# Kernel tuning notes

Measured on AMD Instinct MI355X. Metric: run time of the kernel, lower is better.

The kernel has to match this reference:

```python
import jax, jax.numpy as jnp
import numpy as np

N = 50000
E = 800000
IN_DIM = 512
HID = 512
MLP_HID = 200
N_CLASSES = 2
BN_EPS = 1e-5


def setup_inputs() -> dict:
    key = jax.random.key(0)
    ks = jax.random.split(key, 12)
    def glorot(k, shape):
        fan_in, fan_out = shape[0], shape[1]
        lim = (6.0 / (fan_in + fan_out)) ** 0.5
        return jax.random.uniform(k, shape, jnp.float32, -lim, lim)
    return {
        "features": jax.random.normal(ks[0], (N, IN_DIM), jnp.float32),
        "src": jax.random.randint(ks[1], (E,), 0, N),
        "dst": jax.random.randint(ks[2], (E,), 0, N),
        # SAGEConv layer 1 & 2 (gcn aggregator -> only fc_neigh)
        "W1": glorot(ks[3], (IN_DIM, HID)),
        "b1": jnp.zeros((HID,), jnp.float32),
        "W2": glorot(ks[4], (HID, HID)),
        "b2": jnp.zeros((HID,), jnp.float32),
        # MLP predictor: Linear -> ReLU -> BatchNorm1d -> Linear
        "Wh": glorot(ks[5], (HID, MLP_HID)),
        "bh": jnp.zeros((MLP_HID,), jnp.float32),
        "gamma": jnp.ones((MLP_HID,), jnp.float32),
        "beta": jnp.zeros((MLP_HID,), jnp.float32),
        "Wo": glorot(ks[6], (MLP_HID, N_CLASSES)),
        "bo": jnp.zeros((N_CLASSES,), jnp.float32),
    }


def _sage_gcn_layer(h, src, dst, deg, W, b):
    # dgl.add_self_loop(g) + SAGEConv(aggregator_type='gcn'):
    # neigh_sum over (edges + self-loop) = segment_sum + h;
    # gcn aggregator then adds h_self once more and divides by (in_deg_with_selfloop + 1):
    #   h_neigh = (segment_sum(h[src]) + 2*h) / (deg_orig + 2)
    agg = jax.ops.segment_sum(h[src], dst, num_segments=h.shape[0])
    h_neigh = (agg + 2.0 * h) / (deg + 2.0)[:, None]
    # fc_neigh then activation=relu (fc commutes with the convex aggregation,
    # applied post-aggregation for clarity)
    return jax.nn.relu(h_neigh @ W + b)


def reference(features, src, dst, W1, b1, W2, b2, Wh, bh, gamma, beta, Wo, bo):
    n = features.shape[0]
    deg = jax.ops.segment_sum(jnp.ones_like(src, dtype=features.dtype), dst, num_segments=n)
    h = _sage_gcn_layer(features, src, dst, deg, W1, b1)  # dropout = identity (eval)
    h = _sage_gcn_layer(h, src, dst, deg, W2, b2)
    # MLP predictor (dropout identity): Linear -> ReLU -> BatchNorm1d -> Linear
    h = jax.nn.relu(h @ Wh + bh)
    mean = jnp.mean(h, axis=0)
    var = jnp.var(h, axis=0)  # biased var, matching torch BatchNorm training fwd
    h = (h - mean) * jax.lax.rsqrt(var + BN_EPS) * gamma + beta
    return h @ Wo + bo
```

## Files before the change

### kernel.cpp

```cpp
#include <hip/hip_runtime.h>

#define NN 50000
#define NE 800000
#define DIM 512
#define MLPH 200

typedef __attribute__((ext_vector_type(8))) short short8;
typedef __attribute__((ext_vector_type(4))) float f32x4;
typedef __attribute__((ext_vector_type(4))) unsigned int u32x4;

#define GL2LDS(g, l)                                                     \
    __builtin_amdgcn_global_load_lds(                                    \
        (const __attribute__((address_space(1))) unsigned int*)(g),      \
        (__attribute__((address_space(3))) unsigned int*)(l), 16, 0, 0)

__device__ inline unsigned short f2bf(float f) {
    unsigned int u = __float_as_uint(f);
    unsigned int r = (u + 0x7fffu + ((u >> 16) & 1u)) >> 16;
    return (unsigned short)r;
}
__device__ inline float bflo(unsigned u) { return __uint_as_float(u << 16); }
__device__ inline float bfhi(unsigned u) { return __uint_as_float(u & 0xffff0000u); }
__device__ inline float bf1(unsigned short u) { return __uint_as_float((unsigned)u << 16); }
__device__ inline unsigned pack2(float a, float b) {
    return (unsigned)f2bf(a) | ((unsigned)f2bf(b) << 16);
}

__global__ void k_hist(const int* __restrict__ dst, int* __restrict__ counts) {
    int e = blockIdx.x * blockDim.x + threadIdx.x;
    if (e < NE) atomicAdd(&counts[dst[e]], 1);
}

__global__ void k_part(const int* __restrict__ counts, int* __restrict__ partial) {
    int t = threadIdx.x;
    int i = blockIdx.x * 256 + t;
    int x = (i < NN) ? counts[i] : 0;
#pragma unroll
    for (int off = 32; off; off >>= 1) x += __shfl_down(x, off);
    __shared__ int ws[4];
    if ((t & 63) == 0) ws[t >> 6] = x;
    __syncthreads();
    if (t == 0) partial[blockIdx.x] = ws[0] + ws[1] + ws[2] + ws[3];
}

__global__ void k_scanp(int* __restrict__ partial, int* __restrict__ rowstart, int nb) {
    __shared__ int ws[4];
    int t = threadIdx.x;
    int x = (t < nb) ? partial[t] : 0;
    int v = x;
#pragma unroll
    for (int off = 1; off < 64; off <<= 1) {
        int u = __shfl_up(v, off);
        if ((t & 63) >= off) v += u;
    }
    if ((t & 63) == 63) ws[t >> 6] = v;
    __syncthreads();
    int add = 0;
#pragma unroll
    for (int w = 0; w < 4; w++)
        if (w < (t >> 6)) add += ws[w];
    if (t < nb) partial[t] = v - x + add;
    if (t == 255) rowstart[NN] = v + add;
}

__global__ void k_scan2(const int* __restrict__ counts, const int* __restrict__ pexcl,
                        int* __restrict__ rowstart, int* __restrict__ cursor) {
    __shared__ int ws[4];
    int t = threadIdx.x;
    int i = blockIdx.x * 256 + t;
    int x = (i < NN) ? counts[i] : 0;
    int v = x;
#pragma unroll
    for (int off = 1; off < 64; off <<= 1) {
        int u = __shfl_up(v, off);
        if ((t & 63) >= off) v += u;
    }
    if ((t & 63) == 63) ws[t >> 6] = v;
    __syncthreads();
    int add = 0;
#pragma unroll
    for (int w = 0; w < 4; w++)
        if (w < (t >> 6)) add += ws[w];
    if (i < NN) {
        int r = pexcl[blockIdx.x] + v - x + add;
        rowstart[i] = r;
        cursor[i] = r;
    }
}

__global__ void k_fill(const int* __restrict__ src, const int* __restrict__ dst,
                       int* __restrict__ cursor, int* __restrict__ adj) {
    int e = blockIdx.x * blockDim.x + threadIdx.x;
    if (e < NE) {
        int p = atomicAdd(&cursor[dst[e]], 1);
        adj[p] = src[e];
    }
}

__global__ void k_cvt(const float* __restrict__ in, ushort* __restrict__ out, int n4) {
    int i = blockIdx.x * blockDim.x + threadIdx.x;
    if (i >= n4) return;
    float4 v = *(const float4*)(in + (size_t)i * 4);
    ushort2 a{f2bf(v.x), f2bf(v.y)}, b{f2bf(v.z), f2bf(v.w)};
    *(ushort2*)(out + (size_t)i * 4) = a;
    *(ushort2*)(out + (size_t)i * 4 + 2) = b;
}

__global__ void k_wt3(const float* __restrict__ W1, const float* __restrict__ W2,
                      const float* __restrict__ Wh, ushort* __restrict__ W1t,
                      ushort* __restrict__ W2t, ushort* __restrict__ Wht) {
    int i = blockIdx.x * 256 + threadIdx.x;
    const int S1 = 512 * 512, S2 = 2 * 512 * 512, S3 = 2 * 512 * 512 + MLPH * 512;
    if (i < S1) {
        int n = i >> 9, k = i & 511;
        W1t[i] = f2bf(W1[(size_t)k * 512 + n]);
    } else if (i < S2) {
        int j = i - S1, n = j >> 9, k = j & 511;
        W2t[j] = f2bf(W2[(size_t)k * 512 + n]);
    } else if (i < S3) {
        int j = i - S2, n = j >> 9, k = j & 511;
        Wht[j] = f2bf(Wh[(size_t)k * MLPH + n]);
    }
}

__device__ inline void addrow(float* acc, uint4 v) {
    acc[0] += bflo(v.x); acc[1] += bfhi(v.x);
    acc[2] += bflo(v.y); acc[3] += bfhi(v.y);
    acc[4] += bflo(v.z); acc[5] += bfhi(v.z);
    acc[6] += bflo(v.w); acc[7] += bfhi(v.w);
}

__global__ __launch_bounds__(256) void k_agg_bf(const ushort* __restrict__ h,
                                                const int* __restrict__ rowstart,
                                                const int* __restrict__ adj,
                                                ushort* __restrict__ out) {
    int node = blockIdx.x * 4 + (threadIdx.x >> 6);
    int lane = threadIdx.x & 63;
    if (node >= NN) return;
    int s = rowstart[node], e = rowstart[node + 1];
    const size_t coff = (size_t)lane * 8;
    float acc[8];
    {
        uint4 v = *(const uint4*)(h + (size_t)node * DIM + coff);
        acc[0] = 2.f * bflo(v.x); acc[1] = 2.f * bfhi(v.x);
        acc[2] = 2.f * bflo(v.y); acc[3] = 2.f * bfhi(v.y);
        acc[4] = 2.f * bflo(v.z); acc[5] = 2.f * bfhi(v.z);
        acc[6] = 2.f * bflo(v.w); acc[7] = 2.f * bfhi(v.w);
    }
    int i = s;
    int e4 = s + ((e - s) & ~3);
    for (; i < e4; i += 4) {
        int n0 = adj[i], n1 = adj[i + 1], n2 = adj[i + 2], n3 = adj[i + 3];
        uint4 v0 = *(const uint4*)(h + (size_t)n0 * DIM + coff);
        uint4 v1 = *(const uint4*)(h + (size_t)n1 * DIM + coff);
        uint4 v2 = *(const uint4*)(h + (size_t)n2 * DIM + coff);
        uint4 v3 = *(const uint4*)(h + (size_t)n3 * DIM + coff);
        addrow(acc, v0);
        addrow(acc, v1);
        addrow(acc, v2);
        addrow(acc, v3);
    }
    for (; i < e; i++) {
        int nbr = adj[i];
        uint4 v = *(const uint4*)(h + (size_t)nbr * DIM + coff);
        addrow(acc, v);
    }
    float inv = 1.0f / (float)(e - s + 2);
    u32x4 o;
    o.x = pack2(acc[0] * inv, acc[1] * inv);
    o.y = pack2(acc[2] * inv, acc[3] * inv);
    o.z = pack2(acc[4] * inv, acc[5] * inv);
    o.w = pack2(acc[6] * inv, acc[7] * inv);
    __builtin_nontemporal_store(o, (u32x4*)(out + (size_t)node * DIM + coff));
}

template <int NCOLS, int OMODE>
__global__ __launch_bounds__(512) void k_ggemm(const ushort* __restrict__ A,
                                               const ushort* __restrict__ Bt,
                                               const float* __restrict__ bias,
                                               float* __restrict__ Cf,
                                               ushort* __restrict__ Cb, int M) {
    constexpr int K = 512;
    constexpr int NT = K / 32;
    constexpr int NC = (NCOLS + 127) / 128;
    __shared__ ushort As[3][256 * 32];
    __shared__ ushort Bs[3][128 * 32];
    const int tid = threadIdx.x;
    const int wid = tid >> 6, lane = tid & 63;
    const int wm = wid >> 1, wn = wid & 1;

    const int cpx = gridDim.x >> 3;
    const int wg = (blockIdx.x & 7) * cpx + (blockIdx.x >> 3);
    const int col0 = (wg % NC) * 128;
    const int row0 = (wg / NC) * 256;

    const int l15 = lane & 15, lk = (lane >> 4) * 8;
    const int lrow = lane >> 2;
    const int lseg = (lane & 3) * 8;

    auto stage = [&](int buf, int k0) {
#pragma unroll
        for (int j = 0; j < 2; j++) {
            const int r = wid * 16 + j * 128;
            int gr = row0 + r + lrow;
            if (gr > M - 1) gr = M - 1;
            GL2LDS(A + (size_t)gr * K + k0 + lseg, &As[buf][r * 32]);
        }
        const int rb = wid * 16;
        int gc = col0 + rb + lrow;
        if (NCOLS % 128 != 0) {
            if (gc > NCOLS - 1) gc = NCOLS - 1;
        }
        GL2LDS(Bt + (size_t)gc * K + k0 + lseg, &Bs[buf][rb * 32]);
    };

    f32x4 acc[4][4] = {};
    stage(0, 0);
    stage(1, 32);
    asm volatile("s_waitcnt vmcnt(3)" ::: "memory");
    __builtin_amdgcn_s_barrier();

    for (int t = 0; t < NT; ++t) {
        const int cur = t % 3;
        if (t + 2 < NT) stage((t + 2) % 3, (t + 2) * 32);
        short8 a[4], b[4];
#pragma unroll
        for (int m = 0; m < 4; m++)
            a[m] = *(const short8*)(&As[cur][(wm * 64 + m * 16 + l15) * 32 + lk]);
#pragma unroll
        for (int n = 0; n < 4; n++)
            b[n] = *(const short8*)(&Bs[cur][(wn * 64 + n * 16 + l15) * 32 + lk]);
#pragma unroll
        for (int m = 0; m < 4; m++)
#pragma unroll
            for (int n = 0; n < 4; n++)
                acc[m][n] = __builtin_amdgcn_mfma_f32_16x16x32_bf16(a[m], b[n], acc[m][n], 0, 0, 0);
        if (t + 2 < NT) {
            asm volatile("s_waitcnt vmcnt(3)" ::: "memory");
            __builtin_amdgcn_s_barrier();
        } else if (t + 1 < NT) {
            asm volatile("s_waitcnt vmcnt(0)" ::: "memory");
            __builtin_amdgcn_s_barrier();
        }
    }

    const int crow = row0 + wm * 64;
    const int ccol = col0 + wn * 64;
#pragma unroll
    for (int n = 0; n < 4; n++) {
        int c = ccol + n * 16 + l15;
        if (NCOLS % 128 != 0 && c >= NCOLS) continue;
        float bv = bias[c];
#pragma unroll
        for (int m = 0; m < 4; m++) {
#pragma unroll
            for (int i = 0; i < 4; i++) {
                int r = crow + m * 16 + (lane >> 4) * 4 + i;
                if (r >= M) continue;
                float v = fmaxf(acc[m][n][i] + bv, 0.0f);
                if (OMODE == 0) Cf[(size_t)r * NCOLS + c] = v;
                else Cb[(size_t)r * NCOLS + c] = f2bf(v);
            }
        }
    }
}

__global__ void k_bnstat(const ushort* __restrict__ hm, float* __restrict__ gsum,
                         float* __restrict__ gsq) {
    int j = threadIdx.x;
    if (j >= MLPH) return;
    float s = 0.f, q = 0.f;
    for (int r = blockIdx.x; r < NN; r += gridDim.x) {
        float v = bf1(hm[(size_t)r * MLPH + j]);
        s += v;
        q += v * v;
    }
    atomicAdd(&gsum[j], s);
    atomicAdd(&gsq[j], q);
}

__global__ void k_bnfin(const float* __restrict__ gsum, const float* __restrict__ gsq,
                        const float* __restrict__ gamma, const float* __restrict__ beta,
                        const float* __restrict__ Wo, const float* __restrict__ bo,
                        float* __restrict__ Wo2, float* __restrict__ bo2) {
    __shared__ float sh[MLPH];
    int j = threadIdx.x;
    if (j < MLPH) {
        float mean = gsum[j] / (float)NN;
        float var = gsq[j] / (float)NN - mean * mean;
        float scale = gamma[j] * rsqrtf(var + 1e-5f);
        float shift = beta[j] - mean * scale;
        sh[j] = shift;
        Wo2[j * 2 + 0] = scale * Wo[j * 2 + 0];
        Wo2[j * 2 + 1] = scale * Wo[j * 2 + 1];
    }
    __syncthreads();
    if (j < 2) {
        float acc = bo[j];
        for (int t = 0; t < MLPH; t++) acc += sh[t] * Wo[t * 2 + j];
        bo2[j] = acc;
    }
}

__global__ void k_out(const ushort* __restrict__ hm, const float* __restrict__ Wo2,
                      const float* __restrict__ bo2, float* __restrict__ out) {
    __shared__ float w[MLPH * 2];
    if (threadIdx.x < MLPH * 2) w[threadIdx.x] = Wo2[threadIdx.x];
    __syncthreads();
    int wid = (blockIdx.x * blockDim.x + threadIdx.x) >> 6;
    int lane = threadIdx.x & 63;
    if (wid >= NN) return;
    const ushort* row = hm + (size_t)wid * MLPH;
    float p0 = 0.f, p1 = 0.f;
    for (int j = lane; j < MLPH; j += 64) {
        float v = bf1(row[j]);
        p0 += v * w[j * 2 + 0];
        p1 += v * w[j * 2 + 1];
    }
    for (int off = 32; off; off >>= 1) {
        p0 += __shfl_down(p0, off);
        p1 += __shfl_down(p1, off);
    }
    if (lane == 0) {
        out[wid * 2 + 0] = p0 + bo2[0];
        out[wid * 2 + 1] = p1 + bo2[1];
    }
}

extern "C" void kernel_launch(void* const* d_in, const int* in_sizes, int n_in,
                              void* d_out, int out_size, void* d_ws, size_t ws_size,
                              hipStream_t stream) {
    const float* features = (const float*)d_in[0];
    const int* src = (const int*)d_in[1];
    const int* dst = (const int*)d_in[2];
    const float* W1 = (const float*)d_in[3];
    const float* b1 = (const float*)d_in[4];
    const float* W2 = (const float*)d_in[5];
    const float* b2 = (const float*)d_in[6];
    const float* Wh = (const float*)d_in[7];
    const float* bh = (const float*)d_in[8];
    const float* gamma = (const float*)d_in[9];
    const float* beta = (const float*)d_in[10];
    const float* Wo = (const float*)d_in[11];
    const float* bo = (const float*)d_in[12];
    float* out = (float*)d_out;

    char* w = (char*)d_ws;
    auto alloc = [&](size_t bytes) -> void* {
        void* p = (void*)w;
        w += (bytes + 255) & ~(size_t)255;
        return p;
    };
    ushort* fb = (ushort*)alloc((size_t)NN * DIM * 2);
    ushort* ab = (ushort*)alloc((size_t)NN * DIM * 2);
    ushort* hb = (ushort*)alloc((size_t)NN * DIM * 2);
    ushort* W1t = (ushort*)alloc((size_t)DIM * DIM * 2);
    ushort* W2t = (ushort*)alloc((size_t)DIM * DIM * 2);
    ushort* Wht = (ushort*)alloc((size_t)MLPH * DIM * 2);
    int* adj = (int*)alloc((size_t)NE * 4);
    int* counts = (int*)alloc((size_t)NN * 4);
    int* rowstart = (int*)alloc((size_t)(NN + 1) * 4);
    int* cursor = (int*)alloc((size_t)NN * 4);
    int* partial = (int*)alloc(256 * 4);
    float* gsum = (float*)alloc(MLPH * 4);
    float* gsq = (float*)alloc(MLPH * 4);
    float* Wo2 = (float*)alloc(MLPH * 2 * 4);
    float* bo2 = (float*)alloc(2 * 4);

    hipMemsetAsync(counts, 0, (size_t)NN * 4, stream);
    hipMemsetAsync(gsum, 0, MLPH * 4, stream);
    hipMemsetAsync(gsq, 0, MLPH * 4, stream);

    const int NB = (NN + 255) / 256;

    k_hist<<<(NE + 255) / 256, 256, 0, stream>>>(dst, counts);
    k_part<<<NB, 256, 0, stream>>>(counts, partial);
    k_scanp<<<1, 256, 0, stream>>>(partial, rowstart, NB);
    k_scan2<<<NB, 256, 0, stream>>>(counts, partial, rowstart, cursor);
    k_fill<<<(NE + 255) / 256, 256, 0, stream>>>(src, dst, cursor, adj);

    const int n4 = NN * DIM / 4;
    k_cvt<<<(n4 + 255) / 256, 256, 0, stream>>>(features, fb, n4);
    const int WT = 2 * 512 * 512 + MLPH * 512;
    k_wt3<<<(WT + 255) / 256, 256, 0, stream>>>(W1, W2, Wh, W1t, W2t, Wht);

    const int MBr = (NN + 255) / 256;
    const int G512 = 4 * MBr;
    const int G200 = 2 * MBr;

    k_agg_bf<<<(NN + 3) / 4, 256, 0, stream>>>(fb, rowstart, adj, ab);
    k_ggemm<DIM, 1><<<G512, 512, 0, stream>>>(ab, W1t, b1, nullptr, hb, NN);
    k_agg_bf<<<(NN + 3) / 4, 256, 0, stream>>>(hb, rowstart, adj, ab);
    k_ggemm<DIM, 1><<<G512, 512, 0, stream>>>(ab, W2t, b2, nullptr, fb, NN);
    k_ggemm<MLPH, 1><<<G200, 512, 0, stream>>>(fb, Wht, bh, nullptr, ab, NN);
    k_bnstat<<<512, 256, 0, stream>>>(ab, gsum, gsq);
    k_bnfin<<<1, 256, 0, stream>>>(gsum, gsq, gamma, beta, Wo, bo, Wo2, bo2);
    k_out<<<(NN * 64 + 511) / 512, 512, 0, stream>>>(ab, Wo2, bo2, out);
}
```

Measured before the change: 591.4 us.

## Fuse neighbor aggregation with layer GEMM via shared-memory tile

Replaces the separate aggregation kernel and tiled GEMM with one kernel per SAGE layer. Each block aggregates 64 node rows into an LDS tile, then multiplies that tile by the transposed weights with MFMA, reading B directly from global memory. This removes the round-trip of the aggregated matrix through HBM and one launch per layer. In exchange it gives up the LDS-staged, pipelined B loads of the original GEMM, and the aggregation phase runs serially before the compute phase. The output is written as scalar bf16 stores. The aggregation gather loop is also unrolled by 8 instead of 4.

```diff
diff --git a/kernel.cpp b/kernel.cpp
--- a/kernel.cpp
+++ b/kernel.cpp
@@ -130,48 +130,101 @@
     acc[6] += bflo(v.w); acc[7] += bfhi(v.w);
 }
 
-__global__ __launch_bounds__(256) void k_agg_bf(const ushort* __restrict__ h,
-                                                const int* __restrict__ rowstart,
-                                                const int* __restrict__ adj,
-                                                ushort* __restrict__ out) {
-    int node = blockIdx.x * 4 + (threadIdx.x >> 6);
-    int lane = threadIdx.x & 63;
-    if (node >= NN) return;
-    int s = rowstart[node], e = rowstart[node + 1];
-    const size_t coff = (size_t)lane * 8;
-    float acc[8];
+__global__ __launch_bounds__(512) void k_fused(const ushort* __restrict__ h,
+                                               const int* __restrict__ rowstart,
+                                               const int* __restrict__ adj,
+                                               const ushort* __restrict__ Bt,
+                                               const float* __restrict__ bias,
+                                               ushort* __restrict__ C, int M) {
+    constexpr int K = 512;
+    constexpr int LDP = 520;
+    __shared__ ushort P[64 * LDP];
+    const int tid = threadIdx.x;
+    const int wid = tid >> 6, lane = tid & 63;
+    const int row0 = blockIdx.x * 64;
+
     {
-        uint4 v = *(const uint4*)(h + (size_t)node * DIM + coff);
-        acc[0] = 2.f * bflo(v.x); acc[1] = 2.f * bfhi(v.x);
-        acc[2] = 2.f * bflo(v.y); acc[3] = 2.f * bfhi(v.y);
-        acc[4] = 2.f * bflo(v.z); acc[5] = 2.f * bfhi(v.z);
-        acc[6] = 2.f * bflo(v.w); acc[7] = 2.f * bfhi(v.w);
-    }
-    int i = s;
-    int e4 = s + ((e - s) & ~3);
-    for (; i < e4; i += 4) {
-        int n0 = adj[i], n1 = adj[i + 1], n2 = adj[i + 2], n3 = adj[i + 3];
-        uint4 v0 = *(const uint4*)(h + (size_t)n0 * DIM + coff);
-        uint4 v1 = *(const uint4*)(h + (size_t)n1 * DIM + coff);
-        uint4 v2 = *(const uint4*)(h + (size_t)n2 * DIM + coff);
-        uint4 v3 = *(const uint4*)(h + (size_t)n3 * DIM + coff);
-        addrow(acc, v0);
-        addrow(acc, v1);
-        addrow(acc, v2);
-        addrow(acc, v3);
-    }
-    for (; i < e; i++) {
-        int nbr = adj[i];
-        uint4 v = *(const uint4*)(h + (size_t)nbr * DIM + coff);
-        addrow(acc, v);
-    }
-    float inv = 1.0f / (float)(e - s + 2);
-    u32x4 o;
-    o.x = pack2(acc[0] * inv, acc[1] * inv);
-    o.y = pack2(acc[2] * inv, acc[3] * inv);
-    o.z = pack2(acc[4] * inv, acc[5] * inv);
-    o.w = pack2(acc[6] * inv, acc[7] * inv);
-    __builtin_nontemporal_store(o, (u32x4*)(out + (size_t)node * DIM + coff));
+        const size_t coff = (size_t)lane * 8;
+        for (int i = 0; i < 8; i++) {
+            const int prow = wid * 8 + i;
+            int node = row0 + prow;
+            const int nd = (node < M) ? node : (M - 1);
+            const int s = rowstart[nd], e = rowstart[nd + 1];
+            float acc[8];
+            {
+                uint4 v = *(const uint4*)(h + (size_t)nd * DIM + coff);
+                acc[0] = 2.f * bflo(v.x); acc[1] = 2.f * bfhi(v.x);
+                acc[2] = 2.f * bflo(v.y); acc[3] = 2.f * bfhi(v.y);
+                acc[4] = 2.f * bflo(v.z); acc[5] = 2.f * bfhi(v.z);
+                acc[6] = 2.f * bflo(v.w); acc[7] = 2.f * bfhi(v.w);
+            }
+            int j = s;
+            int e8 = s + ((e - s) & ~7);
+            for (; j < e8; j += 8) {
+                uint4 v0 = *(const uint4*)(h + (size_t)adj[j + 0] * DIM + coff);
+                uint4 v1 = *(const uint4*)(h + (size_t)adj[j + 1] * DIM + coff);
+                uint4 v2 = *(const uint4*)(h + (size_t)adj[j + 2] * DIM + coff);
+                uint4 v3 = *(const uint4*)(h + (size_t)adj[j + 3] * DIM + coff);
+                uint4 v4 = *(const uint4*)(h + (size_t)adj[j + 4] * DIM + coff);
+                uint4 v5 = *(const uint4*)(h + (size_t)adj[j + 5] * DIM + coff);
+                uint4 v6 = *(const uint4*)(h + (size_t)adj[j + 6] * DIM + coff);
+                uint4 v7 = *(const uint4*)(h + (size_t)adj[j + 7] * DIM + coff);
+                addrow(acc, v0); addrow(acc, v1); addrow(acc, v2); addrow(acc, v3);
+                addrow(acc, v4); addrow(acc, v5); addrow(acc, v6); addrow(acc, v7);
+            }
+            for (; j < e; j++) {
+                uint4 v = *(const uint4*)(h + (size_t)adj[j] * DIM + coff);
+                addrow(acc, v);
+            }
+            float inv = 1.0f / (float)(e - s + 2);
+            u32x4 o;
+            o.x = pack2(acc[0] * inv, acc[1] * inv);
+            o.y = pack2(acc[2] * inv, acc[3] * inv);
+            o.z = pack2(acc[4] * inv, acc[5] * inv);
+            o.w = pack2(acc[6] * inv, acc[7] * inv);
+            *(u32x4*)(&P[prow * LDP + lane * 8]) = o;
+        }
+    }
+    __syncthreads();
+
+    const int wm = wid >> 2;
+    const int wn = wid & 3;
+    const int l15 = lane & 15, lk = (lane >> 4) * 8;
+    const ushort* bbase = Bt + (size_t)(wn * 128) * K;
+
+    f32x4 acc[2][8] = {};
+    for (int k0 = 0; k0 < K; k0 += 32) {
+        short8 b[8];
+#pragma unroll
+        for (int n = 0; n < 8; n++)
+            b[n] = *(const short8*)(bbase + (size_t)(n * 16 + l15) * K + k0 + lk);
+        short8 a[2];
+#pragma unroll
+        for (int m = 0; m < 2; m++)
+            a[m] = *(const short8*)(&P[(wm * 32 + m * 16 + l15) * LDP + k0 + lk]);
+#pragma unroll
+        for (int m = 0; m < 2; m++)
+#pragma unroll
+            for (int n = 0; n < 8; n++)
+                acc[m][n] = __builtin_amdgcn_mfma_f32_16x16x32_bf16(a[m], b[n], acc[m][n], 0, 0, 0);
+    }
+
+    const int crow = row0 + wm * 32;
+    const int ccol = wn * 128;
+#pragma unroll
+    for (int n = 0; n < 8; n++) {
+        int c = ccol + n * 16 + l15;
+        float bv = bias[c];
+#pragma unroll
+        for (int m = 0; m < 2; m++) {
+#pragma unroll
+            for (int i = 0; i < 4; i++) {
+                int r = crow + m * 16 + (lane >> 4) * 4 + i;
+                if (r >= M) continue;
+                C[(size_t)r * 512 + c] = f2bf(fmaxf(acc[m][n][i] + bv, 0.0f));
+            }
+        }
+    }
 }
 
 template <int NCOLS, int OMODE>
@@ -352,8 +405,8 @@
         return p;
     };
     ushort* fb = (ushort*)alloc((size_t)NN * DIM * 2);
+    ushort* hb = (ushort*)alloc((size_t)NN * DIM * 2);
     ushort* ab = (ushort*)alloc((size_t)NN * DIM * 2);
-    ushort* hb = (ushort*)alloc((size_t)NN * DIM * 2);
     ushort* W1t = (ushort*)alloc((size_t)DIM * DIM * 2);
     ushort* W2t = (ushort*)alloc((size_t)DIM * DIM * 2);
     ushort* Wht = (ushort*)alloc((size_t)MLPH * DIM * 2);
@@ -384,16 +437,13 @@
     const int WT = 2 * 512 * 512 + MLPH * 512;
     k_wt3<<<(WT + 255) / 256, 256, 0, stream>>>(W1, W2, Wh, W1t, W2t, Wht);
 
-    const int MBr = (NN + 255) / 256;
-    const int G512 = 4 * MBr;
-    const int G200 = 2 * MBr;
-
-    k_agg_bf<<<(NN + 3) / 4, 256, 0, stream>>>(fb, rowstart, adj, ab);
-    k_ggemm<DIM, 1><<<G512, 512, 0, stream>>>(ab, W1t, b1, nullptr, hb, NN);
-    k_agg_bf<<<(NN + 3) / 4, 256, 0, stream>>>(hb, rowstart, adj, ab);
-    k_ggemm<DIM, 1><<<G512, 512, 0, stream>>>(ab, W2t, b2, nullptr, fb, NN);
-    k_ggemm<MLPH, 1><<<G200, 512, 0, stream>>>(fb, Wht, bh, nullptr, ab, NN);
-    k_bnstat<<<512, 256, 0, stream>>>(ab, gsum, gsq);
+    const int FB = (NN + 63) / 64;
+    const int G200 = 2 * NB;
+
+    k_fused<<<FB, 512, 0, stream>>>(fb, rowstart, adj, W1t, b1, hb, NN);
+    k_fused<<<FB, 512, 0, stream>>>(hb, rowstart, adj, W2t, b2, ab, NN);
+    k_ggemm<MLPH, 1><<<G200, 512, 0, stream>>>(ab, Wht, bh, nullptr, hb, NN);
+    k_bnstat<<<512, 256, 0, stream>>>(hb, gsum, gsq);
     k_bnfin<<<1, 256, 0, stream>>>(gsum, gsq, gamma, beta, Wo, bo, Wo2, bo2);
-    k_out<<<(NN * 64 + 511) / 512, 512, 0, stream>>>(ab, Wo2, bo2, out);
-}
+    k_out<<<(NN * 64 + 511) / 512, 512, 0, stream>>>(hb, Wo2, bo2, out);
+}
```

Measured after the change: 819.0 us. 1.38x slower.
